# Performance work log

Hardware: AMD Instinct MI355X
Metric: run time of the kernel (lower is better)

## Reference

```python
import jax, jax.numpy as jnp
import numpy as np

COMMITMENT_LOSS_WEIGHT = 0.25


def setup_inputs() -> dict:
    key = jax.random.key(0)
    k1, k2 = jax.random.split(key)
    B, H, W, C = 64, 32, 32, 256
    D, K = H * W, 1024  # embedding_dim = H*W per the rearrange+reshape in call()
    x = jax.random.normal(k1, (B, H, W, C), dtype=jnp.float32)
    # Orthogonal initializer (like tf.keras.initializers.Orthogonal) via QR
    E = jnp.linalg.qr(jax.random.normal(k2, (D, K), dtype=jnp.float32))[0]
    return {"x": x, "embeddings": E.astype(jnp.float32)}


def reference(x, embeddings):
    B, H, W, C = x.shape
    D = H * W  # embedding_dim
    # einops: 'b h w c -> b c (h w)'
    cont = jnp.transpose(x, (0, 3, 1, 2)).reshape(B, C, D)
    flat = cont.reshape(-1, D)  # [B*C, D]
    # squared L2 distances via norm + matmul (as in get_discretised)
    dists = (jnp.sum(flat * flat, axis=1, keepdims=True)
             + jnp.sum(embeddings * embeddings, axis=0)
             - 2.0 * (flat @ embeddings))  # [B*C, K]
    idx = jnp.argmin(dists, axis=1)  # [B*C]
    # one_hot @ embeddings.T == direct gather of codebook columns
    quantised = embeddings.T[idx].reshape(B, C, D)
    codebook_loss = jnp.mean((jax.lax.stop_gradient(cont) - quantised) ** 2)
    commitment_loss = COMMITMENT_LOSS_WEIGHT * jnp.mean(
        (cont - jax.lax.stop_gradient(quantised)) ** 2)
    loss = codebook_loss + commitment_loss  # layer add_loss terms, summed
    # einops: 'b c (h w) -> b h w c'
    q_bhwc = jnp.transpose(quantised.reshape(B, C, H, W), (0, 2, 3, 1))
    discretised = idx.reshape(-1, C)  # [B, C]
    # straight-through estimator
    q_out = x + jax.lax.stop_gradient(q_bhwc - x)
    return q_out, discretised, loss
```

## Files before the change

### kernel.cpp

```cpp
#include <hip/hip_runtime.h>
#include <float.h>
#include <stdint.h>

#define B_   64
#define C_   256
#define D_   1024
#define K_   1024
#define M_   16384
#define NX_  16777216
#define DISC_OFF NX_
#define LOSS_OFF (NX_ + M_)

typedef _Float16 h8 __attribute__((ext_vector_type(8)));
typedef float    f4 __attribute__((ext_vector_type(4)));

#define XSCALE 512.0f
#define ESCALE 2048.0f
#define DOT_UNSCALE_2 (2.0f / 1048576.0f)

#define WS_EH  0
#define WS_EL  524288
#define WS_CN  1048576
#define WS_PCN 1049600
#define WS_PV  1180672
#define WS_PI  1246208

__device__ __forceinline__ void async16(const _Float16* g, _Float16* l) {
    __builtin_amdgcn_global_load_lds(
        (const __attribute__((address_space(1))) unsigned int*)g,
        (__attribute__((address_space(3))) unsigned int*)l, 16, 0, 0);
}

__global__ __launch_bounds__(256) void split_kernel(const float* __restrict__ x,
                                                    const float* __restrict__ E,
                                                    _Float16* __restrict__ Xh,
                                                    _Float16* __restrict__ Xl,
                                                    _Float16* __restrict__ Eh,
                                                    _Float16* __restrict__ El,
                                                    float* __restrict__ pcn) {
    const int bid = blockIdx.x;
    const int t   = threadIdx.x;
    if (bid < 128) {
        const int o  = bid;
        const int d0 = o * 8;
        const int n0 = t * 4;
        float4 row[8];
        #pragma unroll
        for (int i = 0; i < 8; ++i)
            row[i] = *(const float4*)(E + (size_t)(d0 + i) * K_ + n0);
        float s0 = 0.f, s1 = 0.f, s2 = 0.f, s3 = 0.f;
        h8 hh[4], ll[4];
        #pragma unroll
        for (int i = 0; i < 8; ++i) {
            const float* rp = (const float*)&row[i];
            #pragma unroll
            for (int j = 0; j < 4; ++j) {
                const float v  = rp[j];
                const float vs = v * ESCALE;
                const _Float16 h = (_Float16)vs;
                hh[j][i] = h;
                ll[j][i] = (_Float16)(vs - (float)h);
            }
            s0 = fmaf(rp[0], rp[0], s0);
            s1 = fmaf(rp[1], rp[1], s1);
            s2 = fmaf(rp[2], rp[2], s2);
            s3 = fmaf(rp[3], rp[3], s3);
        }
        float4 sv; sv.x = s0; sv.y = s1; sv.z = s2; sv.w = s3;
        *(float4*)(pcn + o * K_ + n0) = sv;
        const int nt    = n0 >> 4;
        const int kt    = o >> 2;
        const int lane0 = (n0 & 15) + (o & 3) * 16;
        const size_t base = ((size_t)(nt * 32 + kt) * 64 + lane0) * 8;
        #pragma unroll
        for (int j = 0; j < 4; ++j) {
            *(h8*)(Eh + base + (size_t)j * 8) = hh[j];
            *(h8*)(El + base + (size_t)j * 8) = ll[j];
        }
    } else {
        const int tid = (bid - 128) * 256 + t;
        const int o   = tid >> 12;
        const int q   = tid & 4095;
        const int b   = q >> 6;
        const int c0  = (q & 63) * 4;
        const int d0  = o * 8;
        const float* xp = x + ((size_t)(b * 1024 + d0) * 256) + c0;
        float4 row[8];
        #pragma unroll
        for (int i = 0; i < 8; ++i)
            row[i] = *(const float4*)(xp + (size_t)i * 256);
        h8 hh[4], ll[4];
        #pragma unroll
        for (int i = 0; i < 8; ++i) {
            const float* rp = (const float*)&row[i];
            #pragma unroll
            for (int j = 0; j < 4; ++j) {
                const float vs = rp[j] * XSCALE;
                const _Float16 h = (_Float16)vs;
                hh[j][i] = h;
                ll[j][i] = (_Float16)(vs - (float)h);
            }
        }
        const int m     = b * 256 + c0;
        const int mt    = m >> 4;
        const int kt    = o >> 2;
        const int lane0 = (m & 15) + (o & 3) * 16;
        const size_t base = ((size_t)(mt * 32 + kt) * 64 + lane0) * 8;
        #pragma unroll
        for (int j = 0; j < 4; ++j) {
            *(h8*)(Xh + base + (size_t)j * 8) = hh[j];
            *(h8*)(Xl + base + (size_t)j * 8) = ll[j];
        }
    }
}

__global__ __launch_bounds__(256) void colnorm2_kernel(const float* __restrict__ pcn,
                                                       float* __restrict__ cn,
                                                       float* __restrict__ loss_slot) {
    __shared__ float sp[4][64];
    const int t    = threadIdx.x;
    const int col  = blockIdx.x * 64 + (t & 63);
    const int part = t >> 6;
    float s = 0.f;
    #pragma unroll 8
    for (int i = 0; i < 32; ++i) s += pcn[(part * 32 + i) * K_ + col];
    sp[part][t & 63] = s;
    __syncthreads();
    if (t < 64) cn[col] = (sp[0][t] + sp[1][t]) + (sp[2][t] + sp[3][t]);
    if (blockIdx.x == 0 && t == 0) *loss_slot = 0.0f;
}

__global__ __launch_bounds__(512, 2) void gemm_argmin_kernel(
        const _Float16* __restrict__ Xh, const _Float16* __restrict__ Xl,
        const _Float16* __restrict__ Eh, const _Float16* __restrict__ El,
        const float* __restrict__ cn,
        float* __restrict__ pV, int* __restrict__ pI) {
    extern __shared__ _Float16 smem[];
    _Float16* Ab0 = smem;
    _Float16* Ab1 = smem + 8192;
    _Float16* Bb0 = smem + 16384;
    _Float16* Bb1 = smem + 32768;
    float* cV = (float*)(smem + 49152);
    int*   cI = (int*)(cV + 512);

    const int t    = threadIdx.x;
    const int rt   = blockIdx.x >> 2;
    const int ct   = blockIdx.x & 3;
    const int wave = t >> 6, lane = t & 63;
    const int lo16 = lane & 15, hi4 = lane >> 4;
    const int mq   = (wave & 1) * 64;
    const int nq   = (wave >> 1) * 64;
    const int mt0  = rt * 8, nt0 = ct * 16;
    const int n0g  = ct * 256;

    const _Float16* src[6];
    _Float16* dst0[6];
    _Float16* dst1[6];
    #pragma unroll
    for (int i = 0; i < 6; ++i) {
        const int id = wave * 6 + i;
        if (id < 16) {
            const int plane = id >> 3, mt = id & 7;
            src[i]  = (plane ? Xl : Xh) + ((size_t)(mt0 + mt) * 32) * 512 + lane * 8;
            dst0[i] = Ab0 + (plane * 8 + mt) * 512 + lane * 8;
            dst1[i] = Ab1 + (plane * 8 + mt) * 512 + lane * 8;
        } else {
            const int q = id - 16;
            const int plane = q >> 4, nt = q & 15;
            src[i]  = (plane ? El : Eh) + ((size_t)(nt0 + nt) * 32) * 512 + lane * 8;
            dst0[i] = Bb0 + (plane * 16 + nt) * 512 + lane * 8;
            dst1[i] = Bb1 + (plane * 16 + nt) * 512 + lane * 8;
        }
    }

    f4 acc[4][4];
    const f4 zero = {0.f, 0.f, 0.f, 0.f};
    #pragma unroll
    for (int i = 0; i < 4; ++i)
        #pragma unroll
        for (int j = 0; j < 4; ++j) acc[i][j] = zero;

    #pragma unroll
    for (int i = 0; i < 6; ++i) async16(src[i], dst0[i]);

    for (int s = 0; s < 32; ++s) {
        const int cur = s & 1;
        __syncthreads();
        if (s + 1 < 32) {
            #pragma unroll
            for (int i = 0; i < 6; ++i)
                async16(src[i] + (size_t)(s + 1) * 512, cur ? dst0[i] : dst1[i]);
        }
        const _Float16* Abuf = cur ? Ab1 : Ab0;
        const _Float16* Bbuf = cur ? Bb1 : Bb0;

        h8 Bf[2][4];
        #pragma unroll
        for (int tn = 0; tn < 4; ++tn) {
            const int tixn = (nq >> 4) + tn;
            Bf[0][tn] = *(const h8*)&Bbuf[tixn * 512 + lane * 8];
            Bf[1][tn] = *(const h8*)&Bbuf[(16 + tixn) * 512 + lane * 8];
        }
        #pragma unroll
        for (int tm = 0; tm < 4; ++tm) {
            const int tixm = (mq >> 4) + tm;
            const h8 Ah = *(const h8*)&Abuf[tixm * 512 + lane * 8];
            const h8 Al = *(const h8*)&Abuf[(8 + tixm) * 512 + lane * 8];
            #pragma unroll
            for (int tn = 0; tn < 4; ++tn) {
                acc[tm][tn] = __builtin_amdgcn_mfma_f32_16x16x32_f16(Ah, Bf[0][tn], acc[tm][tn], 0, 0, 0);
                acc[tm][tn] = __builtin_amdgcn_mfma_f32_16x16x32_f16(Ah, Bf[1][tn], acc[tm][tn], 0, 0, 0);
                acc[tm][tn] = __builtin_amdgcn_mfma_f32_16x16x32_f16(Al, Bf[0][tn], acc[tm][tn], 0, 0, 0);
            }
        }
    }

    float cnv[4];
    #pragma unroll
    for (int tn = 0; tn < 4; ++tn) cnv[tn] = cn[n0g + nq + tn * 16 + lo16];

    #pragma unroll
    for (int tm = 0; tm < 4; ++tm) {
        #pragma unroll
        for (int r = 0; r < 4; ++r) {
            float bv = FLT_MAX;
            int   bi = 0;
            #pragma unroll
            for (int tn = 0; tn < 4; ++tn) {
                const float v = cnv[tn] - acc[tm][tn][r] * DOT_UNSCALE_2;
                if (v < bv) { bv = v; bi = nq + tn * 16 + lo16; }
            }
            #pragma unroll
            for (int msk = 1; msk < 16; msk <<= 1) {
                const float ov = __shfl_xor(bv, msk, 64);
                const int   oi = __shfl_xor(bi, msk, 64);
                if (ov < bv || (ov == bv && oi < bi)) { bv = ov; bi = oi; }
            }
            if (lo16 == 0) {
                const int row = mq + tm * 16 + hi4 * 4 + r;
                const int g   = wave >> 1;
                cV[row * 4 + g] = bv;
                cI[row * 4 + g] = bi;
            }
        }
    }
    __syncthreads();
    if (t < 128) {
        float bv = FLT_MAX;
        int   bi = 0;
        #pragma unroll
        for (int g = 0; g < 4; ++g) {
            const float v = cV[t * 4 + g];
            const int   i = cI[t * 4 + g];
            if (v < bv || (v == bv && i < bi)) { bv = v; bi = i; }
        }
        const int row = rt * 128 + t;
        pV[row * 4 + ct] = bv;
        pI[row * 4 + ct] = n0g + bi;
    }
}

__global__ __launch_bounds__(256) void reduce_kernel(const float* __restrict__ pV,
                                                     const int* __restrict__ pI,
                                                     float* __restrict__ disc) {
    const int rid = blockIdx.x * 256 + threadIdx.x;
    float bv = FLT_MAX;
    int   bi = 0;
    #pragma unroll
    for (int c = 0; c < 4; ++c) {
        const float v = pV[rid * 4 + c];
        const int   i = pI[rid * 4 + c];
        if (v < bv || (v == bv && i < bi)) { bv = v; bi = i; }
    }
    disc[rid] = (float)bi;
}

__global__ __launch_bounds__(256) void finalize_kernel(const float* __restrict__ x,
                                                       const float* __restrict__ E,
                                                       const float* __restrict__ discf,
                                                       float* __restrict__ out,
                                                       float* __restrict__ loss) {
    __shared__ float Erow[1024];
    const int t = threadIdx.x;
    const int d = blockIdx.x;
    *(float4*)&Erow[t * 4] = *(const float4*)(E + (size_t)d * K_ + t * 4);
    __syncthreads();

    const int bl = t >> 6;
    const int c4 = (t & 63) * 4;
    float lsum = 0.f;
    #pragma unroll 4
    for (int bg = 0; bg < 64; bg += 4) {
        const int b = bg + bl;
        const float4 id4 = *(const float4*)(discf + b * 256 + c4);
        const size_t xoff = ((size_t)(b * 1024 + d) << 8) + c4;
        const float4 xv = *(const float4*)(x + xoff);
        const float e0 = Erow[(int)id4.x];
        const float e1 = Erow[(int)id4.y];
        const float e2 = Erow[(int)id4.z];
        const float e3 = Erow[(int)id4.w];
        float4 qv;
        qv.x = xv.x + (e0 - xv.x);
        qv.y = xv.y + (e1 - xv.y);
        qv.z = xv.z + (e2 - xv.z);
        qv.w = xv.w + (e3 - xv.w);
        *(float4*)(out + xoff) = qv;
        const float d0 = xv.x - e0, d1 = xv.y - e1, d2 = xv.z - e2, d3 = xv.w - e3;
        lsum += fmaf(d0, d0, fmaf(d1, d1, fmaf(d2, d2, d3 * d3)));
    }

    #pragma unroll
    for (int off = 32; off > 0; off >>= 1)
        lsum += __shfl_down(lsum, off);
    __shared__ float wsum[4];
    if ((t & 63) == 0) wsum[t >> 6] = lsum;
    __syncthreads();
    if (t == 0) {
        const float s = (wsum[0] + wsum[1]) + (wsum[2] + wsum[3]);
        atomicAdd(loss, s * (1.25f / 16777216.0f));
    }
}

extern "C" void kernel_launch(void* const* d_in, const int* in_sizes, int n_in,
                              void* d_out, int out_size, void* d_ws, size_t ws_size,
                              hipStream_t stream) {
    (void)in_sizes; (void)n_in; (void)out_size; (void)ws_size;
    const float* x = (const float*)d_in[0];
    const float* E = (const float*)d_in[1];
    float* out = (float*)d_out;
    float* ws  = (float*)d_ws;

    _Float16* Eh = (_Float16*)(ws + WS_EH);
    _Float16* El = (_Float16*)(ws + WS_EL);
    float* cn    = ws + WS_CN;
    float* pcn   = ws + WS_PCN;
    float* pV    = ws + WS_PV;
    int*   pI    = (int*)(ws + WS_PI);

    _Float16* Xh = (_Float16*)out;
    _Float16* Xl = (_Float16*)out + NX_;
    float* disc  = out + DISC_OFF;
    float* loss  = out + LOSS_OFF;

    hipFuncSetAttribute((const void*)gemm_argmin_kernel,
                        hipFuncAttributeMaxDynamicSharedMemorySize, 102400);

    split_kernel   <<<2176, 256, 0, stream>>>(x, E, Xh, Xl, Eh, El, pcn);
    colnorm2_kernel<<<16,   256, 0, stream>>>(pcn, cn, loss);
    gemm_argmin_kernel<<<512, 512, 102400, stream>>>(Xh, Xl, Eh, El, cn, pV, pI);
    reduce_kernel  <<<64,   256, 0, stream>>>(pV, pI, disc);
    finalize_kernel<<<1024, 256, 0, stream>>>(x, E, disc, out, loss);
}
```

Baseline: 258.1 us.

## Fuse x fp16 hi/lo split into GEMM A-tile loading

Removes the separate pass that converted x into split fp16 hi/lo planes in global memory. The GEMM kernel now reads fp32 x directly through registers, splits it, and writes the A tiles to LDS, prefetching the next stage's values during the MFMA loop. This avoids a 64MB read plus 64MB write round trip. In exchange x is re-read by the four column-tile blocks, uses strided scalar loads and ALU work in the GEMM, and adds register pressure.

```diff
diff --git a/kernel.cpp b/kernel.cpp
--- a/kernel.cpp
+++ b/kernel.cpp
@@ -31,86 +31,46 @@
         (__attribute__((address_space(3))) unsigned int*)l, 16, 0, 0);
 }
 
-__global__ __launch_bounds__(256) void split_kernel(const float* __restrict__ x,
-                                                    const float* __restrict__ E,
-                                                    _Float16* __restrict__ Xh,
-                                                    _Float16* __restrict__ Xl,
-                                                    _Float16* __restrict__ Eh,
-                                                    _Float16* __restrict__ El,
-                                                    float* __restrict__ pcn) {
-    const int bid = blockIdx.x;
-    const int t   = threadIdx.x;
-    if (bid < 128) {
-        const int o  = bid;
-        const int d0 = o * 8;
-        const int n0 = t * 4;
-        float4 row[8];
-        #pragma unroll
-        for (int i = 0; i < 8; ++i)
-            row[i] = *(const float4*)(E + (size_t)(d0 + i) * K_ + n0);
-        float s0 = 0.f, s1 = 0.f, s2 = 0.f, s3 = 0.f;
-        h8 hh[4], ll[4];
-        #pragma unroll
-        for (int i = 0; i < 8; ++i) {
-            const float* rp = (const float*)&row[i];
-            #pragma unroll
-            for (int j = 0; j < 4; ++j) {
-                const float v  = rp[j];
-                const float vs = v * ESCALE;
-                const _Float16 h = (_Float16)vs;
-                hh[j][i] = h;
-                ll[j][i] = (_Float16)(vs - (float)h);
-            }
-            s0 = fmaf(rp[0], rp[0], s0);
-            s1 = fmaf(rp[1], rp[1], s1);
-            s2 = fmaf(rp[2], rp[2], s2);
-            s3 = fmaf(rp[3], rp[3], s3);
-        }
-        float4 sv; sv.x = s0; sv.y = s1; sv.z = s2; sv.w = s3;
-        *(float4*)(pcn + o * K_ + n0) = sv;
-        const int nt    = n0 >> 4;
-        const int kt    = o >> 2;
-        const int lane0 = (n0 & 15) + (o & 3) * 16;
-        const size_t base = ((size_t)(nt * 32 + kt) * 64 + lane0) * 8;
+__global__ __launch_bounds__(256) void esplit_kernel(const float* __restrict__ E,
+                                                     _Float16* __restrict__ Eh,
+                                                     _Float16* __restrict__ El,
+                                                     float* __restrict__ pcn) {
+    const int t  = threadIdx.x;
+    const int o  = blockIdx.x;
+    const int d0 = o * 8;
+    const int n0 = t * 4;
+    float4 row[8];
+    #pragma unroll
+    for (int i = 0; i < 8; ++i)
+        row[i] = *(const float4*)(E + (size_t)(d0 + i) * K_ + n0);
+    float s0 = 0.f, s1 = 0.f, s2 = 0.f, s3 = 0.f;
+    h8 hh[4], ll[4];
+    #pragma unroll
+    for (int i = 0; i < 8; ++i) {
+        const float* rp = (const float*)&row[i];
         #pragma unroll
         for (int j = 0; j < 4; ++j) {
-            *(h8*)(Eh + base + (size_t)j * 8) = hh[j];
-            *(h8*)(El + base + (size_t)j * 8) = ll[j];
-        }
-    } else {
-        const int tid = (bid - 128) * 256 + t;
-        const int o   = tid >> 12;
-        const int q   = tid & 4095;
-        const int b   = q >> 6;
-        const int c0  = (q & 63) * 4;
-        const int d0  = o * 8;
-        const float* xp = x + ((size_t)(b * 1024 + d0) * 256) + c0;
-        float4 row[8];
-        #pragma unroll
-        for (int i = 0; i < 8; ++i)
-            row[i] = *(const float4*)(xp + (size_t)i * 256);
-        h8 hh[4], ll[4];
-        #pragma unroll
-        for (int i = 0; i < 8; ++i) {
-            const float* rp = (const float*)&row[i];
-            #pragma unroll
-            for (int j = 0; j < 4; ++j) {
-                const float vs = rp[j] * XSCALE;
-                const _Float16 h = (_Float16)vs;
-                hh[j][i] = h;
-                ll[j][i] = (_Float16)(vs - (float)h);
-            }
-        }
-        const int m     = b * 256 + c0;
-        const int mt    = m >> 4;
-        const int kt    = o >> 2;
-        const int lane0 = (m & 15) + (o & 3) * 16;
-        const size_t base = ((size_t)(mt * 32 + kt) * 64 + lane0) * 8;
-        #pragma unroll
-        for (int j = 0; j < 4; ++j) {
-            *(h8*)(Xh + base + (size_t)j * 8) = hh[j];
-            *(h8*)(Xl + base + (size_t)j * 8) = ll[j];
-        }
+            const float v  = rp[j];
+            const float vs = v * ESCALE;
+            const _Float16 h = (_Float16)vs;
+            hh[j][i] = h;
+            ll[j][i] = (_Float16)(vs - (float)h);
+        }
+        s0 = fmaf(rp[0], rp[0], s0);
+        s1 = fmaf(rp[1], rp[1], s1);
+        s2 = fmaf(rp[2], rp[2], s2);
+        s3 = fmaf(rp[3], rp[3], s3);
+    }
+    float4 sv; sv.x = s0; sv.y = s1; sv.z = s2; sv.w = s3;
+    *(float4*)(pcn + o * K_ + n0) = sv;
+    const int nt    = n0 >> 4;
+    const int kt    = o >> 2;
+    const int lane0 = (n0 & 15) + (o & 3) * 16;
+    const size_t base = ((size_t)(nt * 32 + kt) * 64 + lane0) * 8;
+    #pragma unroll
+    for (int j = 0; j < 4; ++j) {
+        *(h8*)(Eh + base + (size_t)j * 8) = hh[j];
+        *(h8*)(El + base + (size_t)j * 8) = ll[j];
     }
 }
 
@@ -131,7 +91,7 @@
 }
 
 __global__ __launch_bounds__(512, 2) void gemm_argmin_kernel(
-        const _Float16* __restrict__ Xh, const _Float16* __restrict__ Xl,
+        const float* __restrict__ x,
         const _Float16* __restrict__ Eh, const _Float16* __restrict__ El,
         const float* __restrict__ cn,
         float* __restrict__ pV, int* __restrict__ pI) {
@@ -150,28 +110,49 @@
     const int lo16 = lane & 15, hi4 = lane >> 4;
     const int mq   = (wave & 1) * 64;
     const int nq   = (wave >> 1) * 64;
-    const int mt0  = rt * 8, nt0 = ct * 16;
+    const int nt0  = ct * 16;
     const int n0g  = ct * 256;
 
-    const _Float16* src[6];
-    _Float16* dst0[6];
-    _Float16* dst1[6];
-    #pragma unroll
-    for (int i = 0; i < 6; ++i) {
-        const int id = wave * 6 + i;
-        if (id < 16) {
-            const int plane = id >> 3, mt = id & 7;
-            src[i]  = (plane ? Xl : Xh) + ((size_t)(mt0 + mt) * 32) * 512 + lane * 8;
-            dst0[i] = Ab0 + (plane * 8 + mt) * 512 + lane * 8;
-            dst1[i] = Ab1 + (plane * 8 + mt) * 512 + lane * 8;
-        } else {
-            const int q = id - 16;
-            const int plane = q >> 4, nt = q & 15;
-            src[i]  = (plane ? El : Eh) + ((size_t)(nt0 + nt) * 32) * 512 + lane * 8;
-            dst0[i] = Bb0 + (plane * 16 + nt) * 512 + lane * 8;
-            dst1[i] = Bb1 + (plane * 16 + nt) * 512 + lane * 8;
-        }
-    }
+    const _Float16* srcB[4];
+    _Float16* dstB0[4];
+    _Float16* dstB1[4];
+    #pragma unroll
+    for (int i = 0; i < 4; ++i) {
+        const int id = wave * 4 + i;
+        const int plane = id >> 4, nt = id & 15;
+        srcB[i]  = (plane ? El : Eh) + ((size_t)(nt0 + nt) * 32) * 512 + lane * 8;
+        dstB0[i] = Bb0 + (plane * 16 + nt) * 512 + lane * 8;
+        dstB1[i] = Bb1 + (plane * 16 + nt) * 512 + lane * 8;
+    }
+
+    const int b    = rt >> 1;
+    const int c0   = (rt & 1) * 128;
+    const int cl   = t & 127;
+    const int ko8  = t >> 7;
+    const float* xbase = x + ((size_t)(b * 1024 + ko8 * 8)) * 256 + c0 + cl;
+    const int mt    = cl >> 4;
+    const int lane0 = (cl & 15) + ko8 * 16;
+    _Float16* wA[2] = { Ab0 + mt * 512 + lane0 * 8,
+                        Ab1 + mt * 512 + lane0 * 8 };
+
+    float av[8];
+    auto loadA = [&](int s) {
+        #pragma unroll
+        for (int j = 0; j < 8; ++j)
+            av[j] = xbase[((size_t)(s * 32) + j) * 256];
+    };
+    auto writeA = [&](_Float16* w) {
+        h8 hh, ll;
+        #pragma unroll
+        for (int j = 0; j < 8; ++j) {
+            const float vs = av[j] * XSCALE;
+            const _Float16 h = (_Float16)vs;
+            hh[j] = h;
+            ll[j] = (_Float16)(vs - (float)h);
+        }
+        *(h8*)w = hh;
+        *(h8*)(w + 4096) = ll;
+    };
 
     f4 acc[4][4];
     const f4 zero = {0.f, 0.f, 0.f, 0.f};
@@ -181,15 +162,18 @@
         for (int j = 0; j < 4; ++j) acc[i][j] = zero;
 
     #pragma unroll
-    for (int i = 0; i < 6; ++i) async16(src[i], dst0[i]);
+    for (int i = 0; i < 4; ++i) async16(srcB[i], dstB0[i]);
+    loadA(0);
+    writeA(wA[0]);
 
     for (int s = 0; s < 32; ++s) {
         const int cur = s & 1;
         __syncthreads();
         if (s + 1 < 32) {
             #pragma unroll
-            for (int i = 0; i < 6; ++i)
-                async16(src[i] + (size_t)(s + 1) * 512, cur ? dst0[i] : dst1[i]);
+            for (int i = 0; i < 4; ++i)
+                async16(srcB[i] + (size_t)(s + 1) * 512, cur ? dstB0[i] : dstB1[i]);
+            loadA(s + 1);
         }
         const _Float16* Abuf = cur ? Ab1 : Ab0;
         const _Float16* Bbuf = cur ? Bb1 : Bb0;
@@ -213,6 +197,7 @@
                 acc[tm][tn] = __builtin_amdgcn_mfma_f32_16x16x32_f16(Al, Bf[0][tn], acc[tm][tn], 0, 0, 0);
             }
         }
+        if (s + 1 < 32) writeA(cur ? wA[0] : wA[1]);
     }
 
     float cnv[4];
@@ -337,17 +322,15 @@
     float* pV    = ws + WS_PV;
     int*   pI    = (int*)(ws + WS_PI);
 
-    _Float16* Xh = (_Float16*)out;
-    _Float16* Xl = (_Float16*)out + NX_;
     float* disc  = out + DISC_OFF;
     float* loss  = out + LOSS_OFF;
 
     hipFuncSetAttribute((const void*)gemm_argmin_kernel,
                         hipFuncAttributeMaxDynamicSharedMemorySize, 102400);
 
-    split_kernel   <<<2176, 256, 0, stream>>>(x, E, Xh, Xl, Eh, El, pcn);
+    esplit_kernel  <<<128,  256, 0, stream>>>(E, Eh, El, pcn);
     colnorm2_kernel<<<16,   256, 0, stream>>>(pcn, cn, loss);
-    gemm_argmin_kernel<<<512, 512, 102400, stream>>>(Xh, Xl, Eh, El, cn, pV, pI);
+    gemm_argmin_kernel<<<512, 512, 102400, stream>>>(x, Eh, El, cn, pV, pI);
     reduce_kernel  <<<64,   256, 0, stream>>>(pV, pI, disc);
     finalize_kernel<<<1024, 256, 0, stream>>>(x, E, disc, out, loss);
 }
```

Result: faster. 246.5 us (-4.5%).
